# Optimization experiments

Measured on AMD Instinct MI355X. Metric: run time of the kernel, lower is better.

The kernel has to match this reference:

```python
import jax, jax.numpy as jnp
import numpy as np
import math

B, N, M, Lx = 8, 32, 16, 32
D, TE_DIM, IN_DIM, TT = 64, 16, 17, 63   # hid_dim, te_dim, 1+te_dim, hid_dim-1
H, DH, NL = 4, 16, 2
TAU, DELTA = 60.0, 300.0                 # tau, 5 minutes in seconds
P = B * N * M


def _ln(x, g, b):
    mu = x.mean(-1, keepdims=True)
    v = ((x - mu) ** 2).mean(-1, keepdims=True)
    return (x - mu) / jnp.sqrt(v + 1e-5) * g + b


def _time_bias():
    idx = jnp.arange(M)
    dist = jnp.abs(idx[:, None] - idx[None, :]).astype(jnp.float32) * DELTA
    return jnp.log(jnp.exp(-dist / TAU) + 1e-12)


def _pos_enc():
    pos = jnp.arange(M, dtype=jnp.float32)[:, None]
    div = jnp.exp(jnp.arange(0, D, 2, dtype=jnp.float32) * (-math.log(10000.0) / D))
    pe = jnp.zeros((M, D))
    pe = pe.at[:, 0::2].set(jnp.sin(pos * div))
    pe = pe.at[:, 1::2].set(jnp.cos(pos * div))
    return pe


def _heads(t):   # (b, m, D) -> (b, H, m, DH)
    b, m, _ = t.shape
    return t.reshape(b, m, H, DH).transpose(0, 2, 1, 3)


def _merge(t):   # (b, H, m, DH) -> (b, m, D)
    b, _, m, _ = t.shape
    return t.transpose(0, 2, 1, 3).reshape(b, m, D)


def _patch_gattn(x, pm, qw, qb, kw, kb, vw, vb, ow, ob, tbias):
    q, k, v = _heads(x @ qw.T + qb), _heads(x @ kw.T + kb), _heads(x @ vw.T + vb)
    a = jnp.einsum('bhqd,bhkd->bhqk', q, k) / math.sqrt(DH) + tbias[None, None]
    a = jnp.where((pm == 0.0)[:, None, None, :], -1e9, a)
    out = _merge(jnp.einsum('bhqk,bhkd->bhqd', jax.nn.softmax(a, -1), v))
    return (out @ ow.T + ob) * pm[..., None]


def _mha(q_in, kv_in, in_w, in_b, ow, ob, kpm=None):
    wq, wk, wv = in_w[:D], in_w[D:2 * D], in_w[2 * D:]
    bq, bk, bv = in_b[:D], in_b[D:2 * D], in_b[2 * D:]
    q = _heads(q_in @ wq.T + bq)
    k = _heads(kv_in @ wk.T + bk)
    v = _heads(kv_in @ wv.T + bv)
    a = jnp.einsum('bhqd,bhkd->bhqk', q, k) / math.sqrt(DH)
    if kpm is not None:
        a = jnp.where(kpm[:, None, None, :], -1e9, a)
    out = _merge(jnp.einsum('bhqk,bhkd->bhqd', jax.nn.softmax(a, -1), v))
    return out @ ow.T + ob


def _forward(x, mask, ttcn_w1, ttcn_b1, ttcn_w2, ttcn_b2, ttcn_w3, ttcn_b3, t_bias,
             ga_qw, ga_qb, ga_kw, ga_kb, ga_vw, ga_vb, ga_ow, ga_ob,
             tf_in_w, tf_in_b, tf_out_w, tf_out_b, tf_ln1_g, tf_ln1_b, tf_ln2_g, tf_ln2_b,
             tf_fw1, tf_fb1, tf_fw2, tf_fb2,
             q_embed, cls_in_w, cls_in_b, cls_out_w, cls_out_b, logit_w, logit_b):
    m = mask.astype(x.dtype)                          # (P, Lx, 1)
    # --- TTCN: per-sample dynamic filter generation + masked seq-softmax agg ---
    h = jax.nn.relu(x @ ttcn_w1.T + ttcn_b1)
    h = jax.nn.relu(h @ ttcn_w2.T + ttcn_b2)
    filt = h @ ttcn_w3.T + ttcn_b3                    # (P, Lx, IN_DIM*TT)
    filt = filt * m + (1.0 - m) * (-1e8)
    fs = jax.nn.softmax(filt, axis=1).reshape(P, Lx, TT, IN_DIM)
    h_t = jax.nn.relu(jnp.einsum('pli,plti->pt', x, fs) + t_bias)   # (P, TT)
    mask_patch = (m.sum(axis=1) > 0).astype(x.dtype)  # (P, 1)
    xp = jnp.concatenate([h_t, mask_patch], -1).reshape(B, N, M, D)
    pm = mask_patch.reshape(B, N, M)
    tbias = _time_bias()
    pe = _pos_enc()
    xc = xp
    for l in range(NL):
        if l > 0:
            x_last = xc
        xb = xc.reshape(B * N, M, D)
        pmb = pm.reshape(B * N, M)
        xb = xb + _patch_gattn(xb, pmb, ga_qw[l], ga_qb[l], ga_kw[l], ga_kb[l],
                               ga_vw[l], ga_vb[l], ga_ow[l], ga_ob[l], tbias)
        xb = xb + pe[None]
        # post-norm TransformerEncoderLayer (tf_layer = 1, no attn mask, eval mode)
        attn = _mha(xb, xb, tf_in_w[l], tf_in_b[l], tf_out_w[l], tf_out_b[l])
        xb = _ln(xb + attn, tf_ln1_g[l], tf_ln1_b[l])
        ff = jax.nn.relu(xb @ tf_fw1[l].T + tf_fb1[l]) @ tf_fw2[l].T + tf_fb2[l]
        xb = _ln(xb + ff, tf_ln2_g[l], tf_ln2_b[l])
        xc = xb.reshape(B, N, M, D)
        if l > 0:
            xc = x_last + xc
    x_seq = xc.mean(axis=1)                            # (B, M, D)
    kpm = ~((pm > 0).any(axis=1))                      # (B, M), True = padded
    qs = jnp.broadcast_to(q_embed[None], (B, 5, D))
    z = _mha(qs, x_seq, cls_in_w, cls_in_b, cls_out_w, cls_out_b, kpm=kpm)
    return (z @ logit_w.T + logit_b)[..., 0]           # (B, 5)


def setup_inputs() -> dict:
    key = jax.random.key(0)
    ks = iter(jax.random.split(key, 64))
    def rn(shape, s=0.1):
        return jax.random.normal(next(ks), shape, jnp.float32) * s
    inp = {
        'x': jax.random.normal(next(ks), (P, Lx, IN_DIM), jnp.float32),
        'mask': jax.random.randint(next(ks), (P, Lx, 1), 0, 2, jnp.int32),
        'ttcn_w1': rn((TT, IN_DIM)), 'ttcn_b1': jnp.zeros((TT,)),
        'ttcn_w2': rn((TT, TT)), 'ttcn_b2': jnp.zeros((TT,)),
        'ttcn_w3': rn((IN_DIM * TT, TT)), 'ttcn_b3': jnp.zeros((IN_DIM * TT,)),
        't_bias': rn((1, TT)),
        'ga_qw': rn((NL, D, D)), 'ga_qb': jnp.zeros((NL, D)),
        'ga_kw': rn((NL, D, D)), 'ga_kb': jnp.zeros((NL, D)),
        'ga_vw': rn((NL, D, D)), 'ga_vb': jnp.zeros((NL, D)),
        'ga_ow': rn((NL, D, D)), 'ga_ob': jnp.zeros((NL, D)),
        'tf_in_w': rn((NL, 3 * D, D)), 'tf_in_b': jnp.zeros((NL, 3 * D)),
        'tf_out_w': rn((NL, D, D)), 'tf_out_b': jnp.zeros((NL, D)),
        'tf_ln1_g': jnp.ones((NL, D)), 'tf_ln1_b': jnp.zeros((NL, D)),
        'tf_ln2_g': jnp.ones((NL, D)), 'tf_ln2_b': jnp.zeros((NL, D)),
        'tf_fw1': rn((NL, 2048, D)), 'tf_fb1': jnp.zeros((NL, 2048)),
        'tf_fw2': rn((NL, D, 2048)), 'tf_fb2': jnp.zeros((NL, D)),
        'q_embed': rn((5, D), 1.0),
        'cls_in_w': rn((3 * D, D)), 'cls_in_b': jnp.zeros((3 * D,)),
        'cls_out_w': rn((D, D)), 'cls_out_b': jnp.zeros((D,)),
        'logit_w': rn((1, D)), 'logit_b': jnp.zeros((1,)),
    }
    return inp


def reference(x, mask, ttcn_w1, ttcn_b1, ttcn_w2, ttcn_b2, ttcn_w3, ttcn_b3, t_bias,
              ga_qw, ga_qb, ga_kw, ga_kb, ga_vw, ga_vb, ga_ow, ga_ob,
              tf_in_w, tf_in_b, tf_out_w, tf_out_b, tf_ln1_g, tf_ln1_b, tf_ln2_g, tf_ln2_b,
              tf_fw1, tf_fb1, tf_fw2, tf_fb2,
              q_embed, cls_in_w, cls_in_b, cls_out_w, cls_out_b, logit_w, logit_b):
    return _forward(x, mask, ttcn_w1, ttcn_b1, ttcn_w2, ttcn_b2, ttcn_w3, ttcn_b3, t_bias,
                    ga_qw, ga_qb, ga_kw, ga_kb, ga_vw, ga_vb, ga_ow, ga_ob,
                    tf_in_w, tf_in_b, tf_out_w, tf_out_b, tf_ln1_g, tf_ln1_b, tf_ln2_g, tf_ln2_b,
                    tf_fw1, tf_fb1, tf_fw2, tf_fb2,
                    q_embed, cls_in_w, cls_in_b, cls_out_w, cls_out_b, logit_w, logit_b)
```

## Files before the change

### kernel.cpp

```cpp
#include <hip/hip_runtime.h>
#include <hip/hip_bf16.h>
#include <math.h>

#define B_  8
#define N_  32
#define M_  16
#define LX  32
#define D_  64
#define IN_DIM_ 17
#define TT_ 63
#define H_  4
#define DH_ 16
#define P_TOT 4096
#define BN_ 256
#define FF_ 2048

#define FRAG_TOT 83200
#define OFF_INW  2048
#define OFF_OUTW 3584
#define OFF_FW1  4096
#define OFF_FW2  20480

typedef unsigned short ushort_t;
typedef __attribute__((ext_vector_type(8))) short short8;
typedef __attribute__((ext_vector_type(4))) float floatx4;

#define MFMA16(a,b,c) __builtin_amdgcn_mfma_f32_16x16x32_bf16((a),(b),(c),0,0,0)

__device__ __forceinline__ float fast_exp2(float x){
#if __has_builtin(__builtin_amdgcn_exp2f)
  return __builtin_amdgcn_exp2f(x);
#else
  return __expf(x * 0.6931471805599453f);
#endif
}
__device__ __forceinline__ float fast_rcp(float x){
#if __has_builtin(__builtin_amdgcn_rcpf)
  return __builtin_amdgcn_rcpf(x);
#else
  return 1.0f / x;
#endif
}

__device__ __forceinline__ ushort_t f2bf(float f){
  unsigned u = __float_as_uint(f);
  u += 0x7FFFu + ((u >> 16) & 1u);
  return (ushort_t)(u >> 16);
}
__device__ __forceinline__ float bf2f(ushort_t h){ return __uint_as_float(((unsigned)h) << 16); }

__device__ __forceinline__ uint4 pack8(const ushort_t* h){
  uint4 u;
  u.x = (unsigned)h[0] | ((unsigned)h[1] << 16);
  u.y = (unsigned)h[2] | ((unsigned)h[3] << 16);
  u.z = (unsigned)h[4] | ((unsigned)h[5] << 16);
  u.w = (unsigned)h[6] | ((unsigned)h[7] << 16);
  return u;
}

__device__ __forceinline__ void split8(const float* r, short8& hi, short8& lo){
  #pragma unroll
  for (int j = 0; j < 8; ++j){
    float v = r[j];
    ushort_t h = f2bf(v);
    ushort_t l2 = f2bf(v - bf2f(h));
    hi[j] = (short)h; lo[j] = (short)l2;
  }
}
__device__ __forceinline__ uint4 cvt8(const float* r){
  ushort_t hh[8];
  #pragma unroll
  for (int j = 0; j < 8; ++j) hh[j] = f2bf(r[j]);
  return pack8(hh);
}
__device__ __forceinline__ short8 cvt8s(const float* r){
  union { uint4 u4; short8 s8; } cv;
  cv.u4 = cvt8(r);
  return cv.s8;
}

__device__ __forceinline__ floatx4 mm3(short8 ah, short8 al, short8 bh, short8 bl, floatx4 c){
  c = MFMA16(ah, bh, c); c = MFMA16(ah, bl, c); c = MFMA16(al, bh, c); return c;
}

__device__ __forceinline__ float dot64(const float* __restrict__ a, const float* __restrict__ w){
  const float4* a4 = (const float4*)a;
  const float4* w4 = (const float4*)w;
  float acc = 0.f;
  #pragma unroll
  for (int k = 0; k < 16; ++k){ float4 x = a4[k], y = w4[k];
    acc += x.x*y.x + x.y*y.y + x.z*y.z + x.w*y.w; }
  return acc;
}
__device__ __forceinline__ float dot16(const float* __restrict__ a, const float* __restrict__ b){
  const float4* a4 = (const float4*)a; const float4* b4 = (const float4*)b;
  float acc = 0.f;
  #pragma unroll
  for (int k = 0; k < 4; ++k){ float4 x = a4[k], y = b4[k];
    acc += x.x*y.x + x.y*y.y + x.z*y.z + x.w*y.w; }
  return acc;
}

__device__ __forceinline__ void packA68(const float* buf, short8* fA, int tid){
  if (tid < 128){
    int ln = tid & 63, ks = tid >> 6;
    const float* r = buf + (ln & 15)*68 + ks*32 + ((ln >> 4) & 3)*8;
    short8 hi, lo; split8(r, hi, lo);
    fA[tid] = hi; fA[128 + tid] = lo;
  }
}

__global__ __launch_bounds__(256) void prep_kernel(
    const float* __restrict__ w1, const float* __restrict__ w2, const float* __restrict__ w3,
    const float* __restrict__ gqw, const float* __restrict__ gkw,
    const float* __restrict__ gvw, const float* __restrict__ gow,
    const float* __restrict__ inw, const float* __restrict__ outw,
    const float* __restrict__ fw1, const float* __restrict__ fw2,
    uint4* __restrict__ fr)
{
  int s = blockIdx.x*256 + threadIdx.x;
  if (s >= FRAG_TOT) return;
  const float* src; int Nr, Kr, KS, rel; int w3seg = 0, noLo = 0;
  if (s < 256)      { src = w1; Nr=63;  Kr=17; KS=1; rel = s; noLo = 1; }
  else if (s < 768) { src = w2; Nr=63;  Kr=63; KS=2; rel = s-256; noLo = 1; }
  else if (s < 9472){ src = w3; Nr=1071;Kr=63; KS=2; rel = s-768; w3seg = 1; noLo = 1; }
  else {
    int t = s - 9472, l = t / 36864, r2 = t - l*36864;
    if (r2 < 512)        { src = gqw + l*4096;   Nr=64;  Kr=64;   KS=2;  rel = r2; }
    else if (r2 < 1024)  { src = gkw + l*4096;   Nr=64;  Kr=64;   KS=2;  rel = r2-512; }
    else if (r2 < 1536)  { src = gvw + l*4096;   Nr=64;  Kr=64;   KS=2;  rel = r2-1024; }
    else if (r2 < 2048)  { src = gow + l*4096;   Nr=64;  Kr=64;   KS=2;  rel = r2-1536; }
    else if (r2 < 3584)  { src = inw + l*12288;  Nr=192; Kr=64;   KS=2;  rel = r2-2048; }
    else if (r2 < 4096)  { src = outw + l*4096;  Nr=64;  Kr=64;   KS=2;  rel = r2-3584; }
    else if (r2 < 20480) { src = fw1 + l*131072; Nr=2048;Kr=64;   KS=2;  rel = r2-4096; noLo = 1; }
    else                 { src = fw2 + l*131072; Nr=64;  Kr=2048; KS=64; rel = r2-20480; noLo = 1; }
  }
  int lane = rel & 63, tmp = rel >> 6;
  int ks = tmp % KS, nt = tmp / KS;
  int kb = ks*32 + ((lane >> 4) & 3)*8;
  int n, validn;
  if (w3seg){
    int i = nt >> 2, tq = nt & 3;
    int t = tq*16 + (lane & 15);
    n = t*17 + i;
    validn = (t < 63);
  } else {
    n = nt*16 + (lane & 15);
    validn = (n < Nr);
  }
  float v[8];
  #pragma unroll
  for (int j = 0; j < 8; ++j){
    v[j] = (validn && (kb + j) < Kr) ? src[n*Kr + kb + j] : 0.f;
    if (w3seg){
      if ((kb + j) == 63) v[j] = 1.0f;
      v[j] *= 1.4426950408889634f;
    }
  }
  ushort_t hh[8];
  #pragma unroll
  for (int j = 0; j < 8; ++j) hh[j] = f2bf(v[j]);
  fr[s] = pack8(hh);
  if (!noLo){
    ushort_t ll[8];
    #pragma unroll
    for (int j = 0; j < 8; ++j) ll[j] = f2bf(v[j] - bf2f(hh[j]));
    fr[FRAG_TOT + s] = pack8(ll);
  }
}

__global__ __launch_bounds__(256) void ttcn_kernel(
    const float* __restrict__ x, const int* __restrict__ mask,
    const float* __restrict__ b1, const float* __restrict__ b2,
    const float* __restrict__ tb,
    const short8* __restrict__ w1bhi,
    const short8* __restrict__ w2bhi,
    const short8* __restrict__ w3bhi,
    float* __restrict__ xp, float* __restrict__ pm)
{
  __shared__ __align__(16) char pool[16512];
  float*    xs    = (float*)(pool + 0);
  float*    xst   = (float*)(pool + 2560);
  int*      cmap  = (int*)  (pool + 5008);
  float*    xsumv = (float*)(pool + 5136);
  int*      Vp    = (int*)  (pool + 5204);
  short8*   xfhi  = (short8*)(pool + 5216);
  ushort_t* h1t   = (ushort_t*)(pool + 7264);
  ushort_t* h2t   = (ushort_t*)(pool + 11872);

  const int p = blockIdx.x, tid = threadIdx.x;
  const int lane = tid & 63, wvi = tid >> 6;
  const int nidx = lane & 15, quad = lane >> 4;

  for (int idx = tid; idx < LX*IN_DIM_; idx += 256){
    int l = (idx * 3856) >> 16;
    int i = idx - l*17;
    xs[l*20 + i] = x[p*(LX*IN_DIM_) + idx];
  }
  if (tid < 64){
    int mv = (tid < 32) ? mask[p*LX + tid] : 0;
    unsigned long long bal = __ballot(mv != 0);
    if (tid < 32) cmap[tid] = 0;
    int pos = __popcll(bal & ((1ull << tid) - 1ull));
    if (mv != 0) cmap[pos] = tid;
    if (tid == 0) *Vp = (int)__popcll(bal);
  }
  __syncthreads();
  const int V   = *Vp;
  const int two = (V > 16);

  if (tid < 128){
    int mt = tid >> 6;
    if (mt == 0 || two){
      int lc = cmap[mt*16 + nidx];
      float r[8];
      #pragma unroll
      for (int j = 0; j < 8; ++j){
        int k = quad*8 + j;
        r[j] = (k < IN_DIM_) ? xs[lc*20 + k] : 0.f;
      }
      ((uint4*)xfhi)[tid] = cvt8(r);
    }
  } else {
    if (tid < 128 + IN_DIM_){
      int i = tid - 128;
      float s = 0.f;
      #pragma unroll
      for (int l = 0; l < LX; ++l) s += xs[l*20 + i];
      xsumv[i] = s;
    }
    if (two){
      for (int idx = tid - 128; idx < 544; idx += 128){
        int i = idx >> 5, cl = idx & 31;
        xst[i*36 + cl] = xs[cmap[cl]*20 + i];
      }
    } else {
      for (int idx = tid - 128; idx < 272; idx += 128){
        int i = idx >> 4, cl = idx & 15;
        xst[i*36 + cl] = xs[cmap[cl]*20 + i];
      }
    }
  }
  __syncthreads();

  {
    short8 axh0 = xfhi[lane];
    short8 bh = w1bhi[wvi*64 + lane];
    floatx4 a0 = {0.f,0.f,0.f,0.f};
    a0 = MFMA16(axh0, bh, a0);
    int t = wvi*16 + nidx;
    float bb = (t < TT_) ? b1[t] : 0.f;
    if (two){
      short8 axh1 = xfhi[64 + lane];
      floatx4 a1 = {0.f,0.f,0.f,0.f};
      a1 = MFMA16(axh1, bh, a1);
      #pragma unroll
      for (int r = 0; r < 4; ++r)
        h1t[(16+quad*4+r)*72 + t] = f2bf(fmaxf(a1[r] + bb, 0.f));
    }
    #pragma unroll
    for (int r = 0; r < 4; ++r)
      h1t[(quad*4+r)*72 + t] = f2bf(fmaxf(a0[r] + bb, 0.f));
  }
  __syncthreads();

  {
    short8 bh0 = w2bhi[(wvi*2+0)*64 + lane];
    short8 bh1 = w2bhi[(wvi*2+1)*64 + lane];
    short8 a00 = *(const short8*)((const char*)h1t + (nidx*72 + quad*8)*2);
    short8 a01 = *(const short8*)((const char*)h1t + (nidx*72 + 32 + quad*8)*2);
    floatx4 a0 = {0.f,0.f,0.f,0.f};
    a0 = MFMA16(a00, bh0, a0); a0 = MFMA16(a01, bh1, a0);
    int t = wvi*16 + nidx;
    float bb = (t < TT_) ? b2[t] : 0.f;
    if (two){
      short8 a10 = *(const short8*)((const char*)h1t + ((16+nidx)*72 + quad*8)*2);
      short8 a11 = *(const short8*)((const char*)h1t + ((16+nidx)*72 + 32 + quad*8)*2);
      floatx4 a1 = {0.f,0.f,0.f,0.f};
      a1 = MFMA16(a10, bh0, a1); a1 = MFMA16(a11, bh1, a1);
      #pragma unroll
      for (int r = 0; r < 4; ++r)
        h2t[(16+quad*4+r)*72 + t] = f2bf(fmaxf(a1[r] + bb, 0.f));
    }
    #pragma unroll
    for (int r = 0; r < 4; ++r)
      h2t[(quad*4+r)*72 + t] = f2bf(fmaxf(a0[r] + bb, 0.f));
  }
  __syncthreads();

  {
    short8 ah0[2], ah1[2];
    #pragma unroll
    for (int ks = 0; ks < 2; ++ks)
      ah0[ks] = *(const short8*)((const char*)h2t + (nidx*72 + ks*32 + quad*8)*2);
    if (two){
      #pragma unroll
      for (int ks = 0; ks < 2; ++ks)
        ah1[ks] = *(const short8*)((const char*)h2t + ((16+nidx)*72 + ks*32 + quad*8)*2);
    }
    if (quad == 3){
      if (two) ah1[1][7] = (short)((16 + nidx >= V) ? f2bf(-1e8f) : (ushort_t)0);
      else     ah0[1][7] = (short)((nidx >= V)      ? f2bf(-1e8f) : (ushort_t)0);
    }
    const int t_out = wvi*16 + nidx;
    const int rA = quad*4;
    float acc_t = 0.f;
    short8 nbh0 = w3bhi[(wvi*2+0)*64 + lane];
    short8 nbh1 = w3bhi[(wvi*2+1)*64 + lane];
    if (two){
      for (int it = 0; it < 17; ++it){
        short8 bh0 = nbh0, bh1 = nbh1;
        if (it < 16){
          int nt = wvi + it*4 + 4;
          nbh0 = w3bhi[(nt*2+0)*64 + lane];
          nbh1 = w3bhi[(nt*2+1)*64 + lane];
        }
        floatx4 a0 = {0.f,0.f,0.f,0.f}, a1 = {0.f,0.f,0.f,0.f};
        a0 = MFMA16(ah0[0], bh0, a0); a0 = MFMA16(ah0[1], bh1, a0);
        a1 = MFMA16(ah1[0], bh0, a1); a1 = MFMA16(ah1[1], bh1, a1);

        const float4 xA = *(const float4*)(xst + it*36 + rA);
        const float4 xB = *(const float4*)(xst + it*36 + rA + 16);
        float den0 = 0.f, den1 = 0.f, num0 = 0.f, num1 = 0.f;
        float e;
        e = fast_exp2(a0[0]); den0 += e; num0 = fmaf(e, xA.x, num0);
        e = fast_exp2(a0[1]); den0 += e; num0 = fmaf(e, xA.y, num0);
        e = fast_exp2(a0[2]); den0 += e; num0 = fmaf(e, xA.z, num0);
        e = fast_exp2(a0[3]); den0 += e; num0 = fmaf(e, xA.w, num0);
        e = fast_exp2(a1[0]); den1 += e; num1 = fmaf(e, xB.x, num1);
        e = fast_exp2(a1[1]); den1 += e; num1 = fmaf(e, xB.y, num1);
        e = fast_exp2(a1[2]); den1 += e; num1 = fmaf(e, xB.z, num1);
        e = fast_exp2(a1[3]); den1 += e; num1 = fmaf(e, xB.w, num1);
        float den = den0 + den1, num = num0 + num1;
        den += __shfl_xor(den, 16, 64); den += __shfl_xor(den, 32, 64);
        num += __shfl_xor(num, 16, 64); num += __shfl_xor(num, 32, 64);
        float res = (den > 0.f) ? num * fast_rcp(den) : xsumv[it] * (1.f/32.f);
        acc_t += res;
      }
    } else {
      for (int it = 0; it < 17; ++it){
        short8 bh0 = nbh0, bh1 = nbh1;
        if (it < 16){
          int nt = wvi + it*4 + 4;
          nbh0 = w3bhi[(nt*2+0)*64 + lane];
          nbh1 = w3bhi[(nt*2+1)*64 + lane];
        }
        floatx4 a0 = {0.f,0.f,0.f,0.f};
        a0 = MFMA16(ah0[0], bh0, a0); a0 = MFMA16(ah0[1], bh1, a0);

        const float4 xA = *(const float4*)(xst + it*36 + rA);
        float den = 0.f, num = 0.f, e;
        e = fast_exp2(a0[0]); den += e; num = fmaf(e, xA.x, num);
        e = fast_exp2(a0[1]); den += e; num = fmaf(e, xA.y, num);
        e = fast_exp2(a0[2]); den += e; num = fmaf(e, xA.z, num);
        e = fast_exp2(a0[3]); den += e; num = fmaf(e, xA.w, num);
        den += __shfl_xor(den, 16, 64); den += __shfl_xor(den, 32, 64);
        num += __shfl_xor(num, 16, 64); num += __shfl_xor(num, 32, 64);
        float res = (den > 0.f) ? num * fast_rcp(den) : xsumv[it] * (1.f/32.f);
        acc_t += res;
      }
    }
    if (quad == 0 && t_out < TT_)
      xp[p*D_ + t_out] = fmaxf(acc_t + tb[t_out], 0.f);
  }
  if (tid == 0){
    float mp = (V > 0) ? 1.f : 0.f;
    xp[p*D_ + TT_] = mp;
    pm[p] = mp;
  }
}

__global__ __launch_bounds__(256) void layer12_kernel(
    const float* __restrict__ xin, const float* __restrict__ pm,
    const short8* __restrict__ frS,
    const float* __restrict__ gqb, const float* __restrict__ gkb,
    const float* __restrict__ gvb, const float* __restrict__ gob,
    const float* __restrict__ inb, const float* __restrict__ outb,
    const float* __restrict__ ln1g, const float* __restrict__ ln1b,
    const float* __restrict__ fb1, const float* __restrict__ fb2,
    const float* __restrict__ ln2g, const float* __restrict__ ln2b,
    float* __restrict__ xout)
{
  __shared__ __align__(16) float xb[16*68];
  __shared__ __align__(16) float xb2[16*68];
  __shared__ __align__(16) float q_[16*68];
  __shared__ __align__(16) float k_[16*68];
  __shared__ __align__(16) float v_[16*68];
  __shared__ __align__(16) float ao[16*68];
  __shared__ __align__(16) float ss[1024];
  __shared__ __align__(16) short8 fragA[256];
  __shared__ __align__(16) float hbuf[4*16*36];
  __shared__ __align__(16) float part[4*16*68];
  __shared__ __align__(16) float pe_t[1024];
  __shared__ float tbt[16];
  __shared__ float pmv[16], mur[16], rvr[16];

  const int bn = blockIdx.x, tid = threadIdx.x;
  const int lane = tid & 63, wvi = tid >> 6;
  const int nidx = lane & 15, quad = lane >> 4;
  const float* xin_p = xin + bn*1024;

  for (int o = tid; o < 1024; o += 256) xb[(o>>6)*68 + (o&63)] = xin_p[o];
  if (tid < 16) pmv[tid] = pm[bn*16 + tid];
  for (int o = tid; o < 1024; o += 256){
    int tok = o >> 6, d = o & 63;
    float div = __expf((float)(d & ~1) * (-0.14391156831212793f));
    float arg = (float)tok * div;
    pe_t[o] = (d & 1) ? cosf(arg) : sinf(arg);
  }
  if (tid >= 32 && tid < 48) tbt[tid-32] = logf(expf(-5.0f*(float)(tid-32)) + 1e-12f);
  __syncthreads();

  for (int l = 0; l < 2; ++l){
    const int lbase = 9472 + l*36864;
    const float* gqbL = gqb + l*64;  const float* gkbL = gkb + l*64;
    const float* gvbL = gvb + l*64;  const float* gobL = gob + l*64;
    const float* inbL = inb + l*192; const float* outbL = outb + l*64;
    const float* ln1gL = ln1g + l*64; const float* ln1bL = ln1b + l*64;
    const float* fb1L = fb1 + l*2048; const float* fb2L = fb2 + l*64;
    const float* ln2gL = ln2g + l*64; const float* ln2bL = ln2b + l*64;

    float xres[4];
    #pragma unroll
    for (int kk2 = 0; kk2 < 4; ++kk2){
      int o = tid + kk2*256;
      xres[kk2] = xb[(o>>6)*68 + (o&63)];
    }

    short8 gb[3][4], ob4[4], mb[3][4];
    #pragma unroll
    for (int mat = 0; mat < 3; ++mat){
      int base = lbase + mat*512;
      gb[mat][0] = frS[base + (wvi*2+0)*64 + lane];
      gb[mat][1] = frS[FRAG_TOT + base + (wvi*2+0)*64 + lane];
      gb[mat][2] = frS[base + (wvi*2+1)*64 + lane];
      gb[mat][3] = frS[FRAG_TOT + base + (wvi*2+1)*64 + lane];
    }
    {
      int base = lbase + 1536;
      ob4[0] = frS[base + (wvi*2+0)*64 + lane];
      ob4[1] = frS[FRAG_TOT + base + (wvi*2+0)*64 + lane];
      ob4[2] = frS[base + (wvi*2+1)*64 + lane];
      ob4[3] = frS[FRAG_TOT + base + (wvi*2+1)*64 + lane];
    }
    #pragma unroll
    for (int sel = 0; sel < 3; ++sel){
      int base = lbase + OFF_INW + (sel*4 + wvi)*128;
      mb[sel][0] = frS[base + lane];
      mb[sel][1] = frS[FRAG_TOT + base + lane];
      mb[sel][2] = frS[base + 64 + lane];
      mb[sel][3] = frS[FRAG_TOT + base + 64 + lane];
    }

    packA68(xb, fragA, tid);
    __syncthreads();
    {
      short8 axh0 = fragA[lane], axh1 = fragA[64+lane];
      short8 axl0 = fragA[128+lane], axl1 = fragA[192+lane];
      #pragma unroll
      for (int mat = 0; mat < 3; ++mat){
        floatx4 c = {0.f,0.f,0.f,0.f};
        c = mm3(axh0, axl0, gb[mat][0], gb[mat][1], c);
        c = mm3(axh1, axl1, gb[mat][2], gb[mat][3], c);
        int d = wvi*16 + nidx;
        float bb = (mat == 0 ? gqbL : mat == 1 ? gkbL : gvbL)[d];
        float* dst = (mat == 0 ? q_ : mat == 1 ? k_ : v_);
        #pragma unroll
        for (int r = 0; r < 4; ++r) dst[(quad*4+r)*68 + d] = c[r] + bb;
      }
    }
    __syncthreads();
    {
      int row = tid >> 2;
      int h = row >> 4, qm = row & 15;
      int km0 = (tid & 3) * 4;
      float s4[4];
      #pragma unroll
      for (int j = 0; j < 4; ++j){
        int km = km0 + j;
        float acc = dot16(q_ + qm*68 + h*16, k_ + km*68 + h*16);
        int dd = qm - km; if (dd < 0) dd = -dd;
        acc = acc * 0.25f + tbt[dd];
        if (pmv[km] == 0.f) acc = -1e9f;
        s4[j] = acc;
      }
      float mx = fmaxf(fmaxf(s4[0], s4[1]), fmaxf(s4[2], s4[3]));
      mx = fmaxf(mx, __shfl_xor(mx, 1, 64));
      mx = fmaxf(mx, __shfl_xor(mx, 2, 64));
      float e4[4], se = 0.f;
      #pragma unroll
      for (int j = 0; j < 4; ++j){ e4[j] = __expf(s4[j]-mx); se += e4[j]; }
      se += __shfl_xor(se, 1, 64);
      se += __shfl_xor(se, 2, 64);
      float inv = fast_rcp(se);
      #pragma unroll
      for (int j = 0; j < 4; ++j) ss[row*16 + km0 + j] = e4[j]*inv;
    }
    __syncthreads();
    for (int o = tid; o < 1024; o += 256){
      int m = o >> 6, d = o & 63, h = d >> 4;
      float acc = 0.f;
      #pragma unroll
      for (int km = 0; km < 16; ++km) acc += ss[h*256 + m*16 + km] * v_[km*68 + d];
      ao[m*68 + d] = acc;
    }
    __syncthreads();
    packA68(ao, fragA, tid);
    __syncthreads();
    {
      short8 axh0 = fragA[lane], axh1 = fragA[64+lane];
      short8 axl0 = fragA[128+lane], axl1 = fragA[192+lane];
      floatx4 c = {0.f,0.f,0.f,0.f};
      c = mm3(axh0, axl0, ob4[0], ob4[1], c);
      c = mm3(axh1, axl1, ob4[2], ob4[3], c);
      int d = wvi*16 + nidx;
      float bb = gobL[d];
      #pragma unroll
      for (int r = 0; r < 4; ++r){
        int tok = quad*4 + r;
        xb[tok*68 + d] += (c[r] + bb) * pmv[tok] + pe_t[tok*64 + d];
      }
    }
    __syncthreads();

    short8 mob[4], f1c[4], f2c[4];
    {
      int base = lbase + OFF_OUTW;
      mob[0] = frS[base + (wvi*2+0)*64 + lane];
      mob[1] = frS[FRAG_TOT + base + (wvi*2+0)*64 + lane];
      mob[2] = frS[base + (wvi*2+1)*64 + lane];
      mob[3] = frS[FRAG_TOT + base + (wvi*2+1)*64 + lane];
    }
    {
      int f1base = lbase + OFF_FW1, f2base = lbase + OFF_FW2;
      #pragma unroll
      for (int t2 = 0; t2 < 2; ++t2){
        int sb = f1base + ((wvi*32+t2)*2)*64 + lane;
        f1c[t2*2+0] = frS[sb];
        f1c[t2*2+1] = frS[sb + 64];
      }
      #pragma unroll
      for (int ntd = 0; ntd < 4; ++ntd)
        f2c[ntd] = frS[f2base + (ntd*64 + wvi*16)*64 + lane];
    }

    packA68(xb, fragA, tid);
    __syncthreads();
    {
      short8 axh0 = fragA[lane], axh1 = fragA[64+lane];
      short8 axl0 = fragA[128+lane], axl1 = fragA[192+lane];
      #pragma unroll
      for (int sel = 0; sel < 3; ++sel){
        floatx4 c = {0.f,0.f,0.f,0.f};
        c = mm3(axh0, axl0, mb[sel][0], mb[sel][1], c);
        c = mm3(axh1, axl1, mb[sel][2], mb[sel][3], c);
        int d = wvi*16 + nidx;
        float bb = inbL[(sel*4 + wvi)*16 + nidx];
        float* dst = (sel == 0 ? q_ : sel == 1 ? k_ : v_);
        #pragma unroll
        for (int r = 0; r < 4; ++r) dst[(quad*4+r)*68 + d] = c[r] + bb;
      }
    }
    __syncthreads();
    {
      int row = tid >> 2;
      int h = row >> 4, qm = row & 15;
      int km0 = (tid & 3) * 4;
      float s4[4];
      #pragma unroll
      for (int j = 0; j < 4; ++j)
        s4[j] = 0.25f * dot16(q_ + qm*68 + h*16, k_ + (km0+j)*68 + h*16);
      float mx = fmaxf(fmaxf(s4[0], s4[1]), fmaxf(s4[2], s4[3]));
      mx = fmaxf(mx, __shfl_xor(mx, 1, 64));
      mx = fmaxf(mx, __shfl_xor(mx, 2, 64));
      float e4[4], se = 0.f;
      #pragma unroll
      for (int j = 0; j < 4; ++j){ e4[j] = __expf(s4[j]-mx); se += e4[j]; }
      se += __shfl_xor(se, 1, 64);
      se += __shfl_xor(se, 2, 64);
      float inv = fast_rcp(se);
      #pragma unroll
      for (int j = 0; j < 4; ++j) ss[row*16 + km0 + j] = e4[j]*inv;
    }
    __syncthreads();
    for (int o = tid; o < 1024; o += 256){
      int m = o >> 6, d = o & 63, h = d >> 4;
      float acc = 0.f;
      #pragma unroll
      for (int km = 0; km < 16; ++km) acc += ss[h*256 + m*16 + km] * v_[km*68 + d];
      ao[m*68 + d] = acc;
    }
    __syncthreads();
    packA68(ao, fragA, tid);
    __syncthreads();
    {
      short8 axh0 = fragA[lane], axh1 = fragA[64+lane];
      short8 axl0 = fragA[128+lane], axl1 = fragA[192+lane];
      floatx4 c = {0.f,0.f,0.f,0.f};
      c = mm3(axh0, axl0, mob[0], mob[1], c);
      c = mm3(axh1, axl1, mob[2], mob[3], c);
      int d = wvi*16 + nidx;
      float bb = outbL[d];
      #pragma unroll
      for (int r = 0; r < 4; ++r) xb[(quad*4+r)*68 + d] += c[r] + bb;
    }
    __syncthreads();

    if (tid < 64){
      int row = tid >> 2, seg = tid & 3;
      const float* rp = xb + row*68 + seg*16;
      float s = 0.f;
      #pragma unroll
      for (int j = 0; j < 16; ++j) s += rp[j];
      s += __shfl_xor(s, 1, 64); s += __shfl_xor(s, 2, 64);
      float mu = s * (1.f/64.f);
      float v = 0.f;
      #pragma unroll
      for (int j = 0; j < 16; ++j){ float t = rp[j]-mu; v += t*t; }
      v += __shfl_xor(v, 1, 64); v += __shfl_xor(v, 2, 64);
      if (seg == 0){ mur[row] = mu; rvr[row] = rsqrtf(v*(1.f/64.f) + 1e-5f); }
    }
    __syncthreads();
    for (int o = tid; o < 1024; o += 256){
      int m = o >> 6, d = o & 63;
      xb2[m*68 + d] = (xb[m*68 + d] - mur[m]) * rvr[m] * ln1gL[d] + ln1bL[d];
    }
    __syncthreads();
    packA68(xb2, fragA, tid);
    __syncthreads();

    {
      const int w = wvi;
      const int f1base = lbase + OFF_FW1, f2base = lbase + OFF_FW2;
      short8 axh0 = fragA[lane], axh1 = fragA[64 + lane];
      floatx4 y0 = {0.f,0.f,0.f,0.f}, y1 = y0, y2 = y0, y3 = y0;
      float* hw = hbuf + w*576;

      short8 f1n[4], f2n[4];
      for (int it = 0; it < 16; ++it){
        int ntA = w*32 + it*2;
        floatx4 hA = {0.f,0.f,0.f,0.f}, hB = hA;
        hA = MFMA16(axh0, f1c[0], hA); hA = MFMA16(axh1, f1c[1], hA);
        hB = MFMA16(axh0, f1c[2], hB); hB = MFMA16(axh1, f1c[3], hB);
        float bbA = fb1L[ntA*16 + nidx], bbB = fb1L[ntA*16 + 16 + nidx];
        #pragma unroll
        for (int r = 0; r < 4; ++r){
          hw[(quad*4+r)*36 + nidx]      = fmaxf(hA[r] + bbA, 0.f);
          hw[(quad*4+r)*36 + 16 + nidx] = fmaxf(hB[r] + bbB, 0.f);
        }
        if (it < 15){
          int ntN = ntA + 2, kstN = w*16 + it + 1;
          #pragma unroll
          for (int t2 = 0; t2 < 2; ++t2){
            int sb = f1base + ((ntN+t2)*2)*64 + lane;
            f1n[t2*2+0] = frS[sb];
            f1n[t2*2+1] = frS[sb + 64];
          }
          #pragma unroll
          for (int ntd = 0; ntd < 4; ++ntd)
            f2n[ntd] = frS[f2base + (ntd*64 + kstN)*64 + lane];
        }
        short8 ah = cvt8s(hw + (lane & 15)*36 + quad*8);
        y0 = MFMA16(ah, f2c[0], y0);
        y1 = MFMA16(ah, f2c[1], y1);
        y2 = MFMA16(ah, f2c[2], y2);
        y3 = MFMA16(ah, f2c[3], y3);
        #pragma unroll
        for (int j = 0; j < 4; ++j){ f1c[j] = f1n[j]; f2c[j] = f2n[j]; }
      }
      #pragma unroll
      for (int r = 0; r < 4; ++r){
        int row = (quad*4 + r)*68;
        part[w*1088 + row + nidx]      = y0[r];
        part[w*1088 + row + 16 + nidx] = y1[r];
        part[w*1088 + row + 32 + nidx] = y2[r];
        part[w*1088 + row + 48 + nidx] = y3[r];
      }
    }
    __syncthreads();
    for (int o = tid; o < 1024; o += 256){
      int tok = o >> 6, d = o & 63;
      float s = xb2[tok*68 + d] + fb2L[d];
      #pragma unroll
      for (int ww = 0; ww < 4; ++ww) s += part[ww*1088 + tok*68 + d];
      xb[tok*68 + d] = s;
    }
    __syncthreads();
    if (tid < 64){
      int row = tid >> 2, seg = tid & 3;
      const float* rp = xb + row*68 + seg*16;
      float s = 0.f;
      #pragma unroll
      for (int j = 0; j < 16; ++j) s += rp[j];
      s += __shfl_xor(s, 1, 64); s += __shfl_xor(s, 2, 64);
      float mu = s * (1.f/64.f);
      float v = 0.f;
      #pragma unroll
      for (int j = 0; j < 16; ++j){ float t = rp[j]-mu; v += t*t; }
      v += __shfl_xor(v, 1, 64); v += __shfl_xor(v, 2, 64);
      if (seg == 0){ mur[row] = mu; rvr[row] = rsqrtf(v*(1.f/64.f) + 1e-5f); }
    }
    __syncthreads();
    #pragma unroll
    for (int kk2 = 0; kk2 < 4; ++kk2){
      int o = tid + kk2*256;
      int tok = o >> 6, d = o & 63;
      float vv = (xb[tok*68 + d] - mur[tok]) * rvr[tok] * ln2gL[d] + ln2bL[d];
      if (l == 0) xb[tok*68 + d] = vv;
      else        xout[bn*1024 + o] = vv + xres[kk2];
    }
    __syncthreads();
  }
}

__global__ __launch_bounds__(256) void final_kernel(
    const float* __restrict__ xc, const float* __restrict__ pm,
    const float* __restrict__ q_embed,
    const float* __restrict__ cin_w, const float* __restrict__ cin_b,
    const float* __restrict__ cout_w, const float* __restrict__ cout_b,
    const float* __restrict__ logit_w, const float* __restrict__ logit_b,
    float* __restrict__ out)
{
  const int b = blockIdx.x;
  const int tid = threadIdx.x;
  __shared__ __align__(16) float xs[M_ * D_];
  __shared__ float kpmv[M_];
  __shared__ __align__(16) float qv[5 * D_], kv[M_ * D_], vv[M_ * D_];
  __shared__ float sv[H_ * 5 * M_];
  __shared__ __align__(16) float ao[5 * D_], zv[5 * D_];

  for (int o = tid; o < M_ * D_; o += 256) {
    int m = o >> 6, d = o & 63;
    float acc = 0.f;
    #pragma unroll
    for (int n = 0; n < N_; ++n) acc += xc[(((b * N_ + n) * M_ + m) * D_) + d];
    xs[o] = acc * (1.f / 32.f);
  }
  if (tid < M_) {
    float any = 0.f;
    #pragma unroll
    for (int n = 0; n < N_; ++n) any += (pm[(b * N_ + n) * M_ + tid] > 0.f) ? 1.f : 0.f;
    kpmv[tid] = (any > 0.f) ? 0.f : 1.f;
  }
  __syncthreads();

  for (int o = tid; o < 5 * D_; o += 256) {
    int qi = o >> 6, d = o & 63;
    qv[o] = cin_b[d] + dot64(q_embed + qi * D_, cin_w + d * D_);
  }
  for (int o = tid; o < 2 * M_ * D_; o += 256) {
    int sel = o >> 10, r = o & 1023, m = r >> 6, d = r & 63;
    float acc = cin_b[D_ + sel * D_ + d] + dot64(xs + m * D_, cin_w + (D_ + sel * D_ + d) * D_);
    ((sel == 0) ? kv : vv)[r] = acc;
  }
  __syncthreads();

  for (int o = tid; o < H_ * 5 * M_; o += 256) {
    int h = o / 80, r = o % 80, qi = r >> 4, km = r & 15;
    float acc = 0.25f * dot16(qv + qi * D_ + h * DH_, kv + km * D_ + h * DH_);
    if (kpmv[km] != 0.f) acc = -1e9f;
    sv[o] = acc;
  }
  __syncthreads();
  if (tid < H_ * 5) {
    int h = tid / 5, qi = tid % 5;
    float* row = sv + h * 80 + qi * M_;
    float mx = -1e30f;
    #pragma unroll
    for (int km = 0; km < M_; ++km) mx = fmaxf(mx, row[km]);
    float se = 0.f;
    #pragma unroll
    for (int km = 0; km < M_; ++km) { float e = __expf(row[km] - mx); row[km] = e; se += e; }
    float inv = 1.f / se;
    #pragma unroll
    for (int km = 0; km < M_; ++km) row[km] *= inv;
  }
  __syncthreads();
  for (int o = tid; o < 5 * D_; o += 256) {
    int qi = o >> 6, d = o & 63, h = d >> 4;
    float acc = 0.f;
    #pragma unroll
    for (int km = 0; km < M_; ++km) acc += sv[h * 80 + qi * M_ + km] * vv[km * D_ + d];
    ao[o] = acc;
  }
  __syncthreads();
  for (int o = tid; o < 5 * D_; o += 256) {
    int qi = o >> 6, d = o & 63;
    zv[o] = cout_b[d] + dot64(ao + qi * D_, cout_w + d * D_);
  }
  __syncthreads();
  if (tid < 5) {
    float acc = logit_b[0] + dot64(zv + tid * D_, logit_w);
    out[b * 5 + tid] = acc;
  }
}

extern "C" void kernel_launch(void* const* d_in, const int* in_sizes, int n_in,
                              void* d_out, int out_size, void* d_ws, size_t ws_size,
                              hipStream_t stream) {
  const float* x       = (const float*)d_in[0];
  const int*   mask    = (const int*)  d_in[1];
  const float* ttcn_w1 = (const float*)d_in[2];
  const float* ttcn_b1 = (const float*)d_in[3];
  const float* ttcn_w2 = (const float*)d_in[4];
  const float* ttcn_b2 = (const float*)d_in[5];
  const float* ttcn_w3 = (const float*)d_in[6];
  const float* ttcn_b3 = (const float*)d_in[7];
  const float* t_bias  = (const float*)d_in[8];
  const float* ga_qw   = (const float*)d_in[9];
  const float* ga_qb   = (const float*)d_in[10];
  const float* ga_kw   = (const float*)d_in[11];
  const float* ga_kb   = (const float*)d_in[12];
  const float* ga_vw   = (const float*)d_in[13];
  const float* ga_vb   = (const float*)d_in[14];
  const float* ga_ow   = (const float*)d_in[15];
  const float* ga_ob   = (const float*)d_in[16];
  const float* tf_in_w = (const float*)d_in[17];
  const float* tf_in_b = (const float*)d_in[18];
  const float* tf_out_w= (const float*)d_in[19];
  const float* tf_out_b= (const float*)d_in[20];
  const float* tf_ln1g = (const float*)d_in[21];
  const float* tf_ln1b = (const float*)d_in[22];
  const float* tf_ln2g = (const float*)d_in[23];
  const float* tf_ln2b = (const float*)d_in[24];
  const float* tf_fw1  = (const float*)d_in[25];
  const float* tf_fb1  = (const float*)d_in[26];
  const float* tf_fw2  = (const float*)d_in[27];
  const float* tf_fb2  = (const float*)d_in[28];
  const float* q_embed = (const float*)d_in[29];
  const float* cls_in_w  = (const float*)d_in[30];
  const float* cls_in_b  = (const float*)d_in[31];
  const float* cls_out_w = (const float*)d_in[32];
  const float* cls_out_b = (const float*)d_in[33];
  const float* logit_w = (const float*)d_in[34];
  const float* logit_b = (const float*)d_in[35];
  (void)ttcn_b3;

  float* wsf  = (float*)d_ws;
  float* xp   = wsf;
  float* pmb  = wsf + P_TOT * D_;
  float* xbuf = pmb + P_TOT;
  uint4* fr   = (uint4*)(xbuf + P_TOT * D_);
  const short8* frS = (const short8*)fr;

  prep_kernel<<<325, 256, 0, stream>>>(ttcn_w1, ttcn_w2, ttcn_w3,
      ga_qw, ga_kw, ga_vw, ga_ow, tf_in_w, tf_out_w, tf_fw1, tf_fw2, fr);

  ttcn_kernel<<<P_TOT, 256, 0, stream>>>(x, mask, ttcn_b1, ttcn_b2, t_bias,
      frS + 0, frS + 256, frS + 768,
      xp, pmb);

  layer12_kernel<<<BN_, 256, 0, stream>>>(xp, pmb, frS,
      ga_qb, ga_kb, ga_vb, ga_ob, tf_in_b, tf_out_b, tf_ln1g, tf_ln1b,
      tf_fb1, tf_fb2, tf_ln2g, tf_ln2b, xbuf);

  final_kernel<<<B_, 256, 0, stream>>>(xbuf, pmb, q_embed,
                                       cls_in_w, cls_in_b, cls_out_w, cls_out_b,
                                       logit_w, logit_b, (float*)d_out);
}
```

Baseline: 233.2 us.

## Run layer12 kernel with 512 threads and split its matmul and FFN work across 8 waves

Doubles the layer12 block to 8 wavefronts. The 12 Q/K/V projection tiles are spread over 8 waves instead of 3 tiles per wave on 4 waves. Attention scores use 8 threads per row, and the FFN hidden dimension is split across 8 waves with 8-way partial sums. With only 256 blocks, this targets the latency-bound per-block execution by adding wave-level parallelism. The cost is double the hbuf/part shared memory, an 8-way reduction, and idle waves in the output-projection stages. It also relies on packA68 behaving correctly for tid values up to 511.

```diff
diff --git a/kernel.cpp b/kernel.cpp
--- a/kernel.cpp
+++ b/kernel.cpp
@@ -370,7 +370,7 @@
   }
 }
 
-__global__ __launch_bounds__(256) void layer12_kernel(
+__global__ __launch_bounds__(512) void layer12_kernel(
     const float* __restrict__ xin, const float* __restrict__ pm,
     const short8* __restrict__ frS,
     const float* __restrict__ gqb, const float* __restrict__ gkb,
@@ -389,8 +389,8 @@
   __shared__ __align__(16) float ao[16*68];
   __shared__ __align__(16) float ss[1024];
   __shared__ __align__(16) short8 fragA[256];
-  __shared__ __align__(16) float hbuf[4*16*36];
-  __shared__ __align__(16) float part[4*16*68];
+  __shared__ __align__(16) float hbuf[8*16*36];
+  __shared__ __align__(16) float part[8*16*68];
   __shared__ __align__(16) float pe_t[1024];
   __shared__ float tbt[16];
   __shared__ float pmv[16], mur[16], rvr[16];
@@ -400,9 +400,9 @@
   const int nidx = lane & 15, quad = lane >> 4;
   const float* xin_p = xin + bn*1024;
 
-  for (int o = tid; o < 1024; o += 256) xb[(o>>6)*68 + (o&63)] = xin_p[o];
+  for (int o = tid; o < 1024; o += 512) xb[(o>>6)*68 + (o&63)] = xin_p[o];
   if (tid < 16) pmv[tid] = pm[bn*16 + tid];
-  for (int o = tid; o < 1024; o += 256){
+  for (int o = tid; o < 1024; o += 512){
     int tok = o >> 6, d = o & 63;
     float div = __expf((float)(d & ~1) * (-0.14391156831212793f));
     float arg = (float)tok * div;
@@ -420,36 +420,32 @@
     const float* fb1L = fb1 + l*2048; const float* fb2L = fb2 + l*64;
     const float* ln2gL = ln2g + l*64; const float* ln2bL = ln2b + l*64;
 
-    float xres[4];
-    #pragma unroll
-    for (int kk2 = 0; kk2 < 4; ++kk2){
-      int o = tid + kk2*256;
+    float xres[2];
+    #pragma unroll
+    for (int kk2 = 0; kk2 < 2; ++kk2){
+      int o = tid + kk2*512;
       xres[kk2] = xb[(o>>6)*68 + (o&63)];
     }
 
-    short8 gb[3][4], ob4[4], mb[3][4];
-    #pragma unroll
-    for (int mat = 0; mat < 3; ++mat){
-      int base = lbase + mat*512;
-      gb[mat][0] = frS[base + (wvi*2+0)*64 + lane];
-      gb[mat][1] = frS[FRAG_TOT + base + (wvi*2+0)*64 + lane];
-      gb[mat][2] = frS[base + (wvi*2+1)*64 + lane];
-      gb[mat][3] = frS[FRAG_TOT + base + (wvi*2+1)*64 + lane];
-    }
+    short8 gU0[4], gU1[4], mU0[4], mU1[4], ob4[4];
     {
-      int base = lbase + 1536;
-      ob4[0] = frS[base + (wvi*2+0)*64 + lane];
-      ob4[1] = frS[FRAG_TOT + base + (wvi*2+0)*64 + lane];
-      ob4[2] = frS[base + (wvi*2+1)*64 + lane];
-      ob4[3] = frS[FRAG_TOT + base + (wvi*2+1)*64 + lane];
-    }
-    #pragma unroll
-    for (int sel = 0; sel < 3; ++sel){
-      int base = lbase + OFF_INW + (sel*4 + wvi)*128;
-      mb[sel][0] = frS[base + lane];
-      mb[sel][1] = frS[FRAG_TOT + base + lane];
-      mb[sel][2] = frS[base + 64 + lane];
-      mb[sel][3] = frS[FRAG_TOT + base + 64 + lane];
+      int b0 = lbase + wvi*128;
+      gU0[0] = frS[b0 + lane];       gU0[1] = frS[FRAG_TOT + b0 + lane];
+      gU0[2] = frS[b0 + 64 + lane];  gU0[3] = frS[FRAG_TOT + b0 + 64 + lane];
+      int m0 = lbase + OFF_INW + wvi*128;
+      mU0[0] = frS[m0 + lane];       mU0[1] = frS[FRAG_TOT + m0 + lane];
+      mU0[2] = frS[m0 + 64 + lane];  mU0[3] = frS[FRAG_TOT + m0 + 64 + lane];
+      if (wvi < 4){
+        int b1 = lbase + (wvi+8)*128;
+        gU1[0] = frS[b1 + lane];       gU1[1] = frS[FRAG_TOT + b1 + lane];
+        gU1[2] = frS[b1 + 64 + lane];  gU1[3] = frS[FRAG_TOT + b1 + 64 + lane];
+        int m1 = lbase + OFF_INW + (wvi+8)*128;
+        mU1[0] = frS[m1 + lane];       mU1[1] = frS[FRAG_TOT + m1 + lane];
+        mU1[2] = frS[m1 + 64 + lane];  mU1[3] = frS[FRAG_TOT + m1 + 64 + lane];
+        int bo = lbase + 1536 + wvi*128;
+        ob4[0] = frS[bo + lane];       ob4[1] = frS[FRAG_TOT + bo + lane];
+        ob4[2] = frS[bo + 64 + lane];  ob4[3] = frS[FRAG_TOT + bo + 64 + lane];
+      }
     }
 
     packA68(xb, fragA, tid);
@@ -457,47 +453,59 @@
     {
       short8 axh0 = fragA[lane], axh1 = fragA[64+lane];
       short8 axl0 = fragA[128+lane], axl1 = fragA[192+lane];
-      #pragma unroll
-      for (int mat = 0; mat < 3; ++mat){
+      {
+        int u = wvi;
         floatx4 c = {0.f,0.f,0.f,0.f};
-        c = mm3(axh0, axl0, gb[mat][0], gb[mat][1], c);
-        c = mm3(axh1, axl1, gb[mat][2], gb[mat][3], c);
-        int d = wvi*16 + nidx;
-        float bb = (mat == 0 ? gqbL : mat == 1 ? gkbL : gvbL)[d];
-        float* dst = (mat == 0 ? q_ : mat == 1 ? k_ : v_);
+        c = mm3(axh0, axl0, gU0[0], gU0[1], c);
+        c = mm3(axh1, axl1, gU0[2], gU0[3], c);
+        int sel = u >> 2, d = (u & 3)*16 + nidx;
+        float bb = (sel == 0 ? gqbL : gkbL)[d];
+        float* dst = (sel == 0 ? q_ : k_);
         #pragma unroll
         for (int r = 0; r < 4; ++r) dst[(quad*4+r)*68 + d] = c[r] + bb;
       }
+      if (wvi < 4){
+        int u = wvi + 8;
+        floatx4 c = {0.f,0.f,0.f,0.f};
+        c = mm3(axh0, axl0, gU1[0], gU1[1], c);
+        c = mm3(axh1, axl1, gU1[2], gU1[3], c);
+        int d = (u & 3)*16 + nidx;
+        float bb = gvbL[d];
+        #pragma unroll
+        for (int r = 0; r < 4; ++r) v_[(quad*4+r)*68 + d] = c[r] + bb;
+      }
     }
     __syncthreads();
     {
-      int row = tid >> 2;
+      int row = tid >> 3;
       int h = row >> 4, qm = row & 15;
-      int km0 = (tid & 3) * 4;
-      float s4[4];
-      #pragma unroll
-      for (int j = 0; j < 4; ++j){
+      int km0 = (tid & 7) * 2;
+      float s2[2];
+      #pragma unroll
+      for (int j = 0; j < 2; ++j){
         int km = km0 + j;
         float acc = dot16(q_ + qm*68 + h*16, k_ + km*68 + h*16);
         int dd = qm - km; if (dd < 0) dd = -dd;
         acc = acc * 0.25f + tbt[dd];
         if (pmv[km] == 0.f) acc = -1e9f;
-        s4[j] = acc;
-      }
-      float mx = fmaxf(fmaxf(s4[0], s4[1]), fmaxf(s4[2], s4[3]));
+        s2[j] = acc;
+      }
+      float mx = fmaxf(s2[0], s2[1]);
       mx = fmaxf(mx, __shfl_xor(mx, 1, 64));
       mx = fmaxf(mx, __shfl_xor(mx, 2, 64));
-      float e4[4], se = 0.f;
-      #pragma unroll
-      for (int j = 0; j < 4; ++j){ e4[j] = __expf(s4[j]-mx); se += e4[j]; }
+      mx = fmaxf(mx, __shfl_xor(mx, 4, 64));
+      float e2[2], se = 0.f;
+      #pragma unroll
+      for (int j = 0; j < 2; ++j){ e2[j] = __expf(s2[j]-mx); se += e2[j]; }
       se += __shfl_xor(se, 1, 64);
       se += __shfl_xor(se, 2, 64);
+      se += __shfl_xor(se, 4, 64);
       float inv = fast_rcp(se);
       #pragma unroll
-      for (int j = 0; j < 4; ++j) ss[row*16 + km0 + j] = e4[j]*inv;
-    }
-    __syncthreads();
-    for (int o = tid; o < 1024; o += 256){
+      for (int j = 0; j < 2; ++j) ss[row*16 + km0 + j] = e2[j]*inv;
+    }
+    __syncthreads();
+    for (int o = tid; o < 1024; o += 512){
       int m = o >> 6, d = o & 63, h = d >> 4;
       float acc = 0.f;
       #pragma unroll
@@ -507,7 +515,7 @@
     __syncthreads();
     packA68(ao, fragA, tid);
     __syncthreads();
-    {
+    if (wvi < 4){
       short8 axh0 = fragA[lane], axh1 = fragA[64+lane];
       short8 axl0 = fragA[128+lane], axl1 = fragA[192+lane];
       floatx4 c = {0.f,0.f,0.f,0.f};
@@ -524,24 +532,22 @@
     __syncthreads();
 
     short8 mob[4], f1c[4], f2c[4];
-    {
-      int base = lbase + OFF_OUTW;
-      mob[0] = frS[base + (wvi*2+0)*64 + lane];
-      mob[1] = frS[FRAG_TOT + base + (wvi*2+0)*64 + lane];
-      mob[2] = frS[base + (wvi*2+1)*64 + lane];
-      mob[3] = frS[FRAG_TOT + base + (wvi*2+1)*64 + lane];
+    if (wvi < 4){
+      int base = lbase + OFF_OUTW + wvi*128;
+      mob[0] = frS[base + lane];       mob[1] = frS[FRAG_TOT + base + lane];
+      mob[2] = frS[base + 64 + lane];  mob[3] = frS[FRAG_TOT + base + 64 + lane];
     }
     {
       int f1base = lbase + OFF_FW1, f2base = lbase + OFF_FW2;
       #pragma unroll
       for (int t2 = 0; t2 < 2; ++t2){
-        int sb = f1base + ((wvi*32+t2)*2)*64 + lane;
+        int sb = f1base + ((wvi*16+t2)*2)*64 + lane;
         f1c[t2*2+0] = frS[sb];
         f1c[t2*2+1] = frS[sb + 64];
       }
       #pragma unroll
       for (int ntd = 0; ntd < 4; ++ntd)
-        f2c[ntd] = frS[f2base + (ntd*64 + wvi*16)*64 + lane];
+        f2c[ntd] = frS[f2base + (ntd*64 + wvi*8)*64 + lane];
     }
 
     packA68(xb, fragA, tid);
@@ -549,41 +555,53 @@
     {
       short8 axh0 = fragA[lane], axh1 = fragA[64+lane];
       short8 axl0 = fragA[128+lane], axl1 = fragA[192+lane];
-      #pragma unroll
-      for (int sel = 0; sel < 3; ++sel){
+      {
+        int u = wvi;
         floatx4 c = {0.f,0.f,0.f,0.f};
-        c = mm3(axh0, axl0, mb[sel][0], mb[sel][1], c);
-        c = mm3(axh1, axl1, mb[sel][2], mb[sel][3], c);
-        int d = wvi*16 + nidx;
-        float bb = inbL[(sel*4 + wvi)*16 + nidx];
-        float* dst = (sel == 0 ? q_ : sel == 1 ? k_ : v_);
+        c = mm3(axh0, axl0, mU0[0], mU0[1], c);
+        c = mm3(axh1, axl1, mU0[2], mU0[3], c);
+        int sel = u >> 2, d = (u & 3)*16 + nidx;
+        float bb = inbL[u*16 + nidx];
+        float* dst = (sel == 0 ? q_ : k_);
         #pragma unroll
         for (int r = 0; r < 4; ++r) dst[(quad*4+r)*68 + d] = c[r] + bb;
       }
+      if (wvi < 4){
+        int u = wvi + 8;
+        floatx4 c = {0.f,0.f,0.f,0.f};
+        c = mm3(axh0, axl0, mU1[0], mU1[1], c);
+        c = mm3(axh1, axl1, mU1[2], mU1[3], c);
+        int d = (u & 3)*16 + nidx;
+        float bb = inbL[u*16 + nidx];
+        #pragma unroll
+        for (int r = 0; r < 4; ++r) v_[(quad*4+r)*68 + d] = c[r] + bb;
+      }
     }
     __syncthreads();
     {
-      int row = tid >> 2;
+      int row = tid >> 3;
       int h = row >> 4, qm = row & 15;
-      int km0 = (tid & 3) * 4;
-      float s4[4];
-      #pragma unroll
-      for (int j = 0; j < 4; ++j)
-        s4[j] = 0.25f * dot16(q_ + qm*68 + h*16, k_ + (km0+j)*68 + h*16);
-      float mx = fmaxf(fmaxf(s4[0], s4[1]), fmaxf(s4[2], s4[3]));
+      int km0 = (tid & 7) * 2;
+      float s2[2];
+      #pragma unroll
+      for (int j = 0; j < 2; ++j)
+        s2[j] = 0.25f * dot16(q_ + qm*68 + h*16, k_ + (km0+j)*68 + h*16);
+      float mx = fmaxf(s2[0], s2[1]);
       mx = fmaxf(mx, __shfl_xor(mx, 1, 64));
       mx = fmaxf(mx, __shfl_xor(mx, 2, 64));
-      float e4[4], se = 0.f;
-      #pragma unroll
-      for (int j = 0; j < 4; ++j){ e4[j] = __expf(s4[j]-mx); se += e4[j]; }
+      mx = fmaxf(mx, __shfl_xor(mx, 4, 64));
+      float e2[2], se = 0.f;
+      #pragma unroll
+      for (int j = 0; j < 2; ++j){ e2[j] = __expf(s2[j]-mx); se += e2[j]; }
       se += __shfl_xor(se, 1, 64);
       se += __shfl_xor(se, 2, 64);
+      se += __shfl_xor(se, 4, 64);
       float inv = fast_rcp(se);
       #pragma unroll
-      for (int j = 0; j < 4; ++j) ss[row*16 + km0 + j] = e4[j]*inv;
-    }
-    __syncthreads();
-    for (int o = tid; o < 1024; o += 256){
+      for (int j = 0; j < 2; ++j) ss[row*16 + km0 + j] = e2[j]*inv;
+    }
+    __syncthreads();
+    for (int o = tid; o < 1024; o += 512){
       int m = o >> 6, d = o & 63, h = d >> 4;
       float acc = 0.f;
       #pragma unroll
@@ -593,7 +611,7 @@
     __syncthreads();
     packA68(ao, fragA, tid);
     __syncthreads();
-    {
+    if (wvi < 4){
       short8 axh0 = fragA[lane], axh1 = fragA[64+lane];
       short8 axl0 = fragA[128+lane], axl1 = fragA[192+lane];
       floatx4 c = {0.f,0.f,0.f,0.f};
@@ -621,7 +639,7 @@
       if (seg == 0){ mur[row] = mu; rvr[row] = rsqrtf(v*(1.f/64.f) + 1e-5f); }
     }
     __syncthreads();
-    for (int o = tid; o < 1024; o += 256){
+    for (int o = tid; o < 1024; o += 512){
       int m = o >> 6, d = o & 63;
       xb2[m*68 + d] = (xb[m*68 + d] - mur[m]) * rvr[m] * ln1gL[d] + ln1bL[d];
     }
@@ -637,8 +655,8 @@
       float* hw = hbuf + w*576;
 
       short8 f1n[4], f2n[4];
-      for (int it = 0; it < 16; ++it){
-        int ntA = w*32 + it*2;
+      for (int it = 0; it < 8; ++it){
+        int ntA = w*16 + it*2;
         floatx4 hA = {0.f,0.f,0.f,0.f}, hB = hA;
         hA = MFMA16(axh0, f1c[0], hA); hA = MFMA16(axh1, f1c[1], hA);
         hB = MFMA16(axh0, f1c[2], hB); hB = MFMA16(axh1, f1c[3], hB);
@@ -648,8 +666,8 @@
           hw[(quad*4+r)*36 + nidx]      = fmaxf(hA[r] + bbA, 0.f);
           hw[(quad*4+r)*36 + 16 + nidx] = fmaxf(hB[r] + bbB, 0.f);
         }
-        if (it < 15){
-          int ntN = ntA + 2, kstN = w*16 + it + 1;
+        if (it < 7){
+          int ntN = ntA + 2, kstN = w*8 + it + 1;
           #pragma unroll
           for (int t2 = 0; t2 < 2; ++t2){
             int sb = f1base + ((ntN+t2)*2)*64 + lane;
@@ -678,11 +696,11 @@
       }
     }
     __syncthreads();
-    for (int o = tid; o < 1024; o += 256){
+    for (int o = tid; o < 1024; o += 512){
       int tok = o >> 6, d = o & 63;
       float s = xb2[tok*68 + d] + fb2L[d];
       #pragma unroll
-      for (int ww = 0; ww < 4; ++ww) s += part[ww*1088 + tok*68 + d];
+      for (int ww = 0; ww < 8; ++ww) s += part[ww*1088 + tok*68 + d];
       xb[tok*68 + d] = s;
     }
     __syncthreads();
@@ -702,8 +720,8 @@
     }
     __syncthreads();
     #pragma unroll
-    for (int kk2 = 0; kk2 < 4; ++kk2){
-      int o = tid + kk2*256;
+    for (int kk2 = 0; kk2 < 2; ++kk2){
+      int o = tid + kk2*512;
       int tok = o >> 6, d = o & 63;
       float vv = (xb[tok*68 + d] - mur[tok]) * rvr[tok] * ln2gL[d] + ln2bL[d];
       if (l == 0) xb[tok*68 + d] = vv;
@@ -850,7 +868,7 @@
       frS + 0, frS + 256, frS + 768,
       xp, pmb);
 
-  layer12_kernel<<<BN_, 256, 0, stream>>>(xp, pmb, frS,
+  layer12_kernel<<<BN_, 512, 0, stream>>>(xp, pmb, frS,
       ga_qb, ga_kb, ga_vb, ga_ob, tf_in_b, tf_out_b, tf_ln1g, tf_ln1b,
       tf_fb1, tf_fb2, tf_ln2g, tf_ln2b, xbuf);
 
```

After: 229.2 us. Within noise of the previous version (-1.7%).
